# Kernel optimization log

Measured on AMD Instinct MI355X. Metric: run time of the kernel, lower is better.

Reference implementation:

```python
import jax, jax.numpy as jnp
import numpy as np

VOCAB = 50257
D_MODEL = 768
N_LAYERS = 4
N_HEADS = 12
D_HEAD = D_MODEL // N_HEADS
MAX_LEN = 5000
EPS = 1e-5


def _make_pe(max_len, d_model):
    # sinusoidal PE, interleaved sin/cos, base n=10000 (matches PositionalEncodingLayer)
    pos = jnp.arange(max_len, dtype=jnp.float32)[:, None]            # [L,1]
    i = jnp.arange(d_model // 2, dtype=jnp.float32)[None, :]         # [1,D/2]
    theta = pos / jnp.power(10000.0, 2.0 * i / d_model)              # [L,D/2]
    pe = jnp.zeros((max_len, d_model), dtype=jnp.float32)
    pe = pe.at[:, 0::2].set(jnp.sin(theta))
    pe = pe.at[:, 1::2].set(jnp.cos(theta))
    return pe


def setup_inputs() -> dict:
    key = jax.random.key(0)
    ks = jax.random.split(key, 10)
    B, S = 2, 1024
    tokens = jax.random.randint(ks[0], (B, S), 0, VOCAB)
    std = 0.02
    embed = jax.random.normal(ks[1], (VOCAB, D_MODEL), jnp.float32) * std
    pe = _make_pe(MAX_LEN, D_MODEL)
    # per-layer stacked params, torch nn.Linear convention: y = x @ W.T + b
    wq_w = jax.random.normal(ks[2], (N_LAYERS, D_MODEL, D_MODEL), jnp.float32) * std
    wk_w = jax.random.normal(ks[3], (N_LAYERS, D_MODEL, D_MODEL), jnp.float32) * std
    wv_w = jax.random.normal(ks[4], (N_LAYERS, D_MODEL, D_MODEL), jnp.float32) * std
    lin_w = jax.random.normal(ks[5], (N_LAYERS, D_MODEL, D_MODEL), jnp.float32) * std
    wq_b = jnp.zeros((N_LAYERS, D_MODEL), jnp.float32)
    wk_b = jnp.zeros((N_LAYERS, D_MODEL), jnp.float32)
    wv_b = jnp.zeros((N_LAYERS, D_MODEL), jnp.float32)
    lin_b = jnp.zeros((N_LAYERS, D_MODEL), jnp.float32)
    n1_s = jnp.ones((N_LAYERS, D_MODEL), jnp.float32)
    n1_b = jnp.zeros((N_LAYERS, D_MODEL), jnp.float32)
    n2_s = jnp.ones((N_LAYERS, D_MODEL), jnp.float32)
    n2_b = jnp.zeros((N_LAYERS, D_MODEL), jnp.float32)
    unembed_w = jax.random.normal(ks[6], (VOCAB, D_MODEL), jnp.float32) * std
    unembed_b = jnp.zeros((VOCAB,), jnp.float32)
    return dict(tokens=tokens, embed=embed, pe=pe,
                wq_w=wq_w, wq_b=wq_b, wk_w=wk_w, wk_b=wk_b, wv_w=wv_w, wv_b=wv_b,
                lin_w=lin_w, lin_b=lin_b, n1_s=n1_s, n1_b=n1_b, n2_s=n2_s, n2_b=n2_b,
                unembed_w=unembed_w, unembed_b=unembed_b)


def _layernorm(x, scale, bias):
    m = jnp.mean(x, axis=-1, keepdims=True)
    v = jnp.mean(jnp.square(x - m), axis=-1, keepdims=True)
    return (x - m) * jax.lax.rsqrt(v + EPS) * scale + bias


def _attn_block(x, wq_w, wq_b, wk_w, wk_b, wv_w, wv_b, lin_w, lin_b, n1_s, n1_b, n2_s, n2_b):
    B, S, D = x.shape
    def proj(w, b):
        y = x @ w.T + b
        return y.reshape(B, S, N_HEADS, D_HEAD).transpose(0, 2, 1, 3)  # [B,H,S,Dh]
    q, k, v = proj(wq_w, wq_b), proj(wk_w, wk_b), proj(wv_w, wv_b)
    scores = jnp.einsum('bhqd,bhkd->bhqk', q, k) / jnp.sqrt(jnp.float32(D_HEAD))
    causal = jnp.tril(jnp.ones((S, S), dtype=bool))
    scores = jnp.where(causal, scores, -jnp.inf)
    probs = jax.nn.softmax(scores, axis=-1)
    attn = jnp.einsum('bhqk,bhkd->bhqd', probs, v)
    attn = attn.transpose(0, 2, 1, 3).reshape(B, S, D)
    x = _layernorm(x + attn, n1_s, n1_b)
    x = _layernorm(x + (x @ lin_w.T + lin_b), n2_s, n2_b)
    return x


def reference(tokens, embed, pe, wq_w, wq_b, wk_w, wk_b, wv_w, wv_b,
              lin_w, lin_b, n1_s, n1_b, n2_s, n2_b, unembed_w, unembed_b):
    B, S = tokens.shape
    x = embed[tokens] + pe[:S]
    for l in range(N_LAYERS):
        x = _attn_block(x, wq_w[l], wq_b[l], wk_w[l], wk_b[l], wv_w[l], wv_b[l],
                        lin_w[l], lin_b[l], n1_s[l], n1_b[l], n2_s[l], n2_b[l])
    logits = x @ unembed_w.T + unembed_b
    return logits
```

## Files before the change

kernel.cpp:

```cpp
#include <hip/hip_runtime.h>
#include <hip/hip_bf16.h>


#define VOCAB 50257
#define DM 768
#define NL 4
#define NH 12
#define DH 64
#define SEQ 1024
#define BATCH 2
#define ROWS (BATCH * SEQ)
#define QKVN (3 * DM)

typedef __attribute__((ext_vector_type(8))) short short8;
typedef __attribute__((ext_vector_type(4))) float f32x4;

__device__ __forceinline__ unsigned short f2bf(float f) {
    union { float f; unsigned u; } v; v.f = f;
    unsigned r = v.u + 0x7FFFu + ((v.u >> 16) & 1u);
    return (unsigned short)(r >> 16);
}

#define GLOAD16(gp, lp)                                                        \
    __builtin_amdgcn_global_load_lds(                                          \
        (const __attribute__((address_space(1))) unsigned int*)(gp),           \
        (__attribute__((address_space(3))) unsigned int*)(lp), 16, 0, 0)

#define BARRIER() asm volatile("s_barrier" ::: "memory")
#define VMCNT0()  asm volatile("s_waitcnt vmcnt(0)" ::: "memory")

__global__ __launch_bounds__(256) void cvt_kernel(const float* __restrict__ in,
                                                  unsigned short* __restrict__ out,
                                                  int n4) {
    int i = blockIdx.x * 256 + threadIdx.x;
    if (i < n4) {
        float4 v = ((const float4*)in)[i];
        ushort4 o;
        o.x = f2bf(v.x); o.y = f2bf(v.y); o.z = f2bf(v.z); o.w = f2bf(v.w);
        ((ushort4*)out)[i] = o;
    }
}

__global__ __launch_bounds__(256) void cvt_qkv_kernel(const float* __restrict__ wq,
                                                      const float* __restrict__ wk,
                                                      const float* __restrict__ wv,
                                                      unsigned short* __restrict__ dst,
                                                      int n4) {
    int i = blockIdx.x * 256 + threadIdx.x;
    if (i >= n4) return;
    const int PER_L = 3 * DM * DM / 4, PER_W = DM * DM / 4;
    int l = i / PER_L;
    int rem = i - l * PER_L;
    int w = rem / PER_W;
    int r2 = rem - w * PER_W;
    const float* src = (w == 0) ? wq : (w == 1) ? wk : wv;
    float4 v = ((const float4*)src)[(size_t)l * PER_W + r2];
    ushort4 o;
    o.x = f2bf(v.x); o.y = f2bf(v.y); o.z = f2bf(v.z); o.w = f2bf(v.w);
    ((ushort4*)dst)[i] = o;
}

__global__ __launch_bounds__(256) void pack_qkv_bias(const float* __restrict__ bq,
                                                     const float* __restrict__ bk,
                                                     const float* __restrict__ bv,
                                                     float* __restrict__ dst) {
    int i = blockIdx.x * 256 + threadIdx.x;
    if (i >= NL * QKVN) return;
    int l = i / QKVN, c = i - l * QKVN;
    int w = c / DM, cc = c - w * DM;
    const float* src = (w == 0) ? bq : (w == 1) ? bk : bv;
    dst[i] = src[l * DM + cc];
}

__global__ __launch_bounds__(256) void embed_kernel(const int* __restrict__ tok,
                                                    const float* __restrict__ emb,
                                                    const float* __restrict__ pe,
                                                    float* __restrict__ xf,
                                                    unsigned short* __restrict__ xb) {
    int row = blockIdx.x;
    int t = tok[row];
    int s = row & (SEQ - 1);
    #pragma unroll
    for (int j = 0; j < 3; ++j) {
        int c = threadIdx.x + j * 256;
        float v = emb[(size_t)t * DM + c] + pe[(size_t)s * DM + c];
        xf[(size_t)row * DM + c] = v;
        xb[(size_t)row * DM + c] = f2bf(v);
    }
}

__global__ __launch_bounds__(256) void ln_kernel(const float* __restrict__ A,
                                                 const float* __restrict__ Bi,
                                                 const float* __restrict__ sc,
                                                 const float* __restrict__ bi,
                                                 float* __restrict__ xf,
                                                 unsigned short* __restrict__ xb) {
    const int w = threadIdx.x >> 6, lane = threadIdx.x & 63;
    const int row = blockIdx.x * 4 + w;
    const float* ap = A + (size_t)row * DM;
    const float* bp = Bi + (size_t)row * DM;
    float4 v[3];
    float sum = 0.f;
    #pragma unroll
    for (int j = 0; j < 3; ++j) {
        int c4 = lane * 3 + j;
        float4 a4 = ((const float4*)ap)[c4];
        float4 b4 = ((const float4*)bp)[c4];
        v[j].x = a4.x + b4.x; v[j].y = a4.y + b4.y;
        v[j].z = a4.z + b4.z; v[j].w = a4.w + b4.w;
        sum += (v[j].x + v[j].y) + (v[j].z + v[j].w);
    }
    #pragma unroll
    for (int off = 32; off > 0; off >>= 1) sum += __shfl_xor(sum, off);
    float mean = sum * (1.f / DM);
    float vs = 0.f;
    #pragma unroll
    for (int j = 0; j < 3; ++j) {
        float dx = v[j].x - mean, dy = v[j].y - mean, dz = v[j].z - mean, dw = v[j].w - mean;
        vs += dx * dx + dy * dy + dz * dz + dw * dw;
    }
    #pragma unroll
    for (int off = 32; off > 0; off >>= 1) vs += __shfl_xor(vs, off);
    float rstd = rsqrtf(vs * (1.f / DM) + 1e-5f);
    #pragma unroll
    for (int j = 0; j < 3; ++j) {
        int c4 = lane * 3 + j;
        float4 s4 = ((const float4*)sc)[c4];
        float4 b4 = ((const float4*)bi)[c4];
        float4 o;
        o.x = (v[j].x - mean) * rstd * s4.x + b4.x;
        o.y = (v[j].y - mean) * rstd * s4.y + b4.y;
        o.z = (v[j].z - mean) * rstd * s4.z + b4.z;
        o.w = (v[j].w - mean) * rstd * s4.w + b4.w;
        ((float4*)(xf + (size_t)row * DM))[c4] = o;
        ushort4 h;
        h.x = f2bf(o.x); h.y = f2bf(o.y); h.z = f2bf(o.z); h.w = f2bf(o.w);
        ((ushort4*)(xb + (size_t)row * DM))[c4] = h;
    }
}

template <int OUT_BF16>
__global__ __launch_bounds__(256, 5) void gemm64h(const unsigned short* __restrict__ A,
                                                  const unsigned short* __restrict__ B,
                                                  const float* __restrict__ bias,
                                                  void* __restrict__ C,
                                                  int M, int N, int K, int gx) {
    __shared__ __align__(16) unsigned short As[2][64 * 64];
    __shared__ __align__(16) unsigned short Bs[2][64 * 64];
    int bid = blockIdx.x;
    const int nwg = gridDim.x;
    if ((nwg & 7) == 0) {
        int q = nwg >> 3;
        bid = (bid & 7) * q + (bid >> 3);
    }
    const int bx = bid % gx, by = bid / gx;
    const int m0 = bx * 64, n0 = by * 64;
    const int tid = threadIdx.x, lane = tid & 63, wid = tid >> 6;
    const int wm = wid >> 1, wn = wid & 1;
    const int lr = lane & 15, lq = lane >> 4;

    const int sr = tid >> 3;
    const int sch = tid & 7;
    const int scs = sch ^ (sr & 7);
    const unsigned short* aP[2];
    const unsigned short* bP[2];
    int sO[2];
    #pragma unroll
    for (int i = 0; i < 2; ++i) {
        int r = sr + i * 32;
        aP[i] = A + (size_t)(m0 + r) * K + scs * 8;
        int br = n0 + r; if (br >= N) br = N - 1;
        bP[i] = B + (size_t)br * K + scs * 8;
        sO[i] = r * 64 + sch * 8;
    }

#define STG(t, c)                                                              \
    do { _Pragma("unroll")                                                     \
        for (int _i = 0; _i < 2; ++_i)                                         \
            GLOAD16(aP[_i] + (t) * 64, &As[c][sO[_i]]);                        \
        _Pragma("unroll")                                                      \
        for (int _i = 0; _i < 2; ++_i)                                         \
            GLOAD16(bP[_i] + (t) * 64, &Bs[c][sO[_i]]);                        \
    } while (0)

    f32x4 acc[2][2] = {};
    const int NT = K >> 6;

    STG(0, 0);
    VMCNT0();
    BARRIER();

    int cur = 0;
    for (int t = 0; t < NT; ++t) {
        if (t + 1 < NT) STG(t + 1, cur ^ 1);
        #pragma unroll
        for (int kk = 0; kk < 2; ++kk) {
            short8 a[2], b[2];
            #pragma unroll
            for (int i = 0; i < 2; ++i) {
                int ar = wm * 32 + i * 16 + lr;
                a[i] = *reinterpret_cast<const short8*>(
                    &As[cur][ar * 64 + (((kk * 4 + lq) ^ (ar & 7)) * 8)]);
                int br = wn * 32 + i * 16 + lr;
                b[i] = *reinterpret_cast<const short8*>(
                    &Bs[cur][br * 64 + (((kk * 4 + lq) ^ (br & 7)) * 8)]);
            }
            #pragma unroll
            for (int i = 0; i < 2; ++i)
                #pragma unroll
                for (int j = 0; j < 2; ++j)
                    acc[i][j] = __builtin_amdgcn_mfma_f32_16x16x32_bf16(a[i], b[j], acc[i][j], 0, 0, 0);
        }
        VMCNT0();
        BARRIER();
        cur ^= 1;
    }

    #pragma unroll
    for (int i = 0; i < 2; ++i) {
        int row = m0 + wm * 32 + i * 16 + lq * 4;
        #pragma unroll
        for (int j = 0; j < 2; ++j) {
            int col = n0 + wn * 32 + j * 16 + lr;
            if (col < N) {
                float bv = bias[col];
                #pragma unroll
                for (int r = 0; r < 4; ++r) {
                    float v = acc[i][j][r] + bv;
                    if (OUT_BF16) ((unsigned short*)C)[(size_t)(row + r) * N + col] = f2bf(v);
                    else          ((float*)C)[(size_t)(row + r) * N + col] = v;
                }
            }
        }
    }
#undef STG
}

__global__ __launch_bounds__(256) void attn_kernel(const unsigned short* __restrict__ Q,
                                                   const unsigned short* __restrict__ K,
                                                   const unsigned short* __restrict__ V,
                                                   int ld,
                                                   float* __restrict__ O) {
    __shared__ __align__(16) unsigned short Ks[64 * 64];
    __shared__ __align__(16) unsigned short Vs[64 * 64];
    __shared__ __align__(16) unsigned short Ps[4][16 * 64];
    const int qb = blockIdx.x;
    const int bh = blockIdx.y;
    const int b = bh / NH, h = bh % NH;
    const int tid = threadIdx.x, lane = tid & 63, w = tid >> 6;
    const int lr = lane & 15, lq = lane >> 4;
    const int wq0 = qb * 64 + w * 16;
    const size_t base = (size_t)b * SEQ * ld + h * DH;
    const size_t obase = (size_t)b * SEQ * DM + h * DH;

    short8 qf[2];
    {
        const unsigned short* qp = Q + base + (size_t)(wq0 + lr) * ld + lq * 8;
        qf[0] = *reinterpret_cast<const short8*>(qp);
        qf[1] = *reinterpret_cast<const short8*>(qp + 32);
    }
    f32x4 o_acc[4] = {};
    float mrow[4], lrow[4];
    #pragma unroll
    for (int r = 0; r < 4; ++r) { mrow[r] = -1e30f; lrow[r] = 0.f; }

    const int srow = tid >> 3, scol = (tid & 7) * 8;
    for (int t = 0; t <= qb; ++t) {
        const int kv0 = t * 64;
        #pragma unroll
        for (int rr = 0; rr < 2; ++rr) {
            int row = rr * 32 + srow;
            {
                const unsigned short* kp = K + base + (size_t)(kv0 + row) * ld + scol;
                short8 v = *reinterpret_cast<const short8*>(kp);
                *reinterpret_cast<short8*>(&Ks[(row * 64 + scol) ^ ((row & 7) << 3)]) = v;
            }
            {
                const unsigned short* vp = V + base + (size_t)(kv0 + row) * ld + scol;
                short8 v = *reinterpret_cast<const short8*>(vp);
                #pragma unroll
                for (int j = 0; j < 8; ++j) {
                    int d = scol + j;
                    Vs[(d * 64 + row) ^ ((d & 7) << 3)] = (unsigned short)v[j];
                }
            }
        }
        __syncthreads();
        if (kv0 <= wq0 + 15) {
            f32x4 s[4];
            #pragma unroll
            for (int n = 0; n < 4; ++n) {
                int br = n * 16 + lr;
                short8 b0 = *reinterpret_cast<const short8*>(&Ks[(br * 64 + lq * 8) ^ ((br & 7) << 3)]);
                short8 b1 = *reinterpret_cast<const short8*>(&Ks[(br * 64 + 32 + lq * 8) ^ ((br & 7) << 3)]);
                f32x4 z = {};
                z = __builtin_amdgcn_mfma_f32_16x16x32_bf16(qf[0], b0, z, 0, 0, 0);
                z = __builtin_amdgcn_mfma_f32_16x16x32_bf16(qf[1], b1, z, 0, 0, 0);
                s[n] = z;
            }
            const bool diag = (t == qb);
            #pragma unroll
            for (int n = 0; n < 4; ++n)
                #pragma unroll
                for (int r = 0; r < 4; ++r) {
                    float v = s[n][r] * 0.125f;
                    if (diag) {
                        int rg = wq0 + lq * 4 + r;
                        int cg = kv0 + n * 16 + lr;
                        if (cg > rg) v = -1e30f;
                    }
                    s[n][r] = v;
                }
            float f[4];
            #pragma unroll
            for (int r = 0; r < 4; ++r) {
                float mx = fmaxf(fmaxf(s[0][r], s[1][r]), fmaxf(s[2][r], s[3][r]));
                #pragma unroll
                for (int off = 1; off < 16; off <<= 1) mx = fmaxf(mx, __shfl_xor(mx, off));
                float mn = fmaxf(mrow[r], mx);
                f[r] = exp2f((mrow[r] - mn) * 1.44269504f);
                mrow[r] = mn;
            }
            #pragma unroll
            for (int n = 0; n < 4; ++n)
                #pragma unroll
                for (int r = 0; r < 4; ++r)
                    s[n][r] = exp2f((s[n][r] - mrow[r]) * 1.44269504f);
            #pragma unroll
            for (int r = 0; r < 4; ++r) {
                float ls = ((s[0][r] + s[1][r]) + (s[2][r] + s[3][r]));
                #pragma unroll
                for (int off = 1; off < 16; off <<= 1) ls += __shfl_xor(ls, off);
                lrow[r] = lrow[r] * f[r] + ls;
            }
            #pragma unroll
            for (int n = 0; n < 4; ++n)
                #pragma unroll
                for (int r = 0; r < 4; ++r) {
                    int pr = lq * 4 + r, pc = n * 16 + lr;
                    Ps[w][(pr * 64 + pc) ^ ((pr & 7) << 3)] = f2bf(s[n][r]);
                }
            #pragma unroll
            for (int n = 0; n < 4; ++n)
                #pragma unroll
                for (int r = 0; r < 4; ++r) o_acc[n][r] *= f[r];
            #pragma unroll
            for (int kk = 0; kk < 2; ++kk) {
                short8 pa = *reinterpret_cast<const short8*>(
                    &Ps[w][(lr * 64 + kk * 32 + lq * 8) ^ ((lr & 7) << 3)]);
                #pragma unroll
                for (int n = 0; n < 4; ++n) {
                    int vr = n * 16 + lr;
                    short8 bv = *reinterpret_cast<const short8*>(
                        &Vs[(vr * 64 + kk * 32 + lq * 8) ^ ((vr & 7) << 3)]);
                    o_acc[n] = __builtin_amdgcn_mfma_f32_16x16x32_bf16(pa, bv, o_acc[n], 0, 0, 0);
                }
            }
        }
        __syncthreads();
    }
    #pragma unroll
    for (int r = 0; r < 4; ++r) {
        float inv = 1.f / lrow[r];
        int row = wq0 + lq * 4 + r;
        #pragma unroll
        for (int n = 0; n < 4; ++n)
            O[obase + (size_t)row * DM + n * 16 + lr] = o_acc[n][r] * inv;
    }
}

extern "C" void kernel_launch(void* const* d_in, const int* in_sizes, int n_in,
                              void* d_out, int out_size, void* d_ws, size_t ws_size,
                              hipStream_t stream) {
    const int*   tokens   = (const int*)d_in[0];
    const float* embed    = (const float*)d_in[1];
    const float* pe       = (const float*)d_in[2];
    const float* wq_w     = (const float*)d_in[3];
    const float* wq_b     = (const float*)d_in[4];
    const float* wk_w     = (const float*)d_in[5];
    const float* wk_b     = (const float*)d_in[6];
    const float* wv_w     = (const float*)d_in[7];
    const float* wv_b     = (const float*)d_in[8];
    const float* lin_w    = (const float*)d_in[9];
    const float* lin_b    = (const float*)d_in[10];
    const float* n1_s     = (const float*)d_in[11];
    const float* n1_b     = (const float*)d_in[12];
    const float* n2_s     = (const float*)d_in[13];
    const float* n2_b     = (const float*)d_in[14];
    const float* unemb_w  = (const float*)d_in[15];
    const float* unemb_b  = (const float*)d_in[16];

    char* ws = (char*)d_ws;
    size_t off = 0;
    auto carve = [&](size_t bytes) { char* p = ws + off; off += (bytes + 255) & ~(size_t)255; return p; };
    float*          xf     = (float*)carve((size_t)ROWS * DM * 4);
    float*          yb     = (float*)carve((size_t)ROWS * DM * 4);
    unsigned short* xb     = (unsigned short*)carve((size_t)ROWS * DM * 2);
    unsigned short* qkv    = (unsigned short*)carve((size_t)ROWS * QKVN * 2);
    unsigned short* wqkv_h = (unsigned short*)carve((size_t)NL * QKVN * DM * 2);
    unsigned short* lin_h  = (unsigned short*)carve((size_t)NL * DM * DM * 2);
    unsigned short* ue_h   = (unsigned short*)carve((size_t)VOCAB * DM * 2);
    float*          qkvb   = (float*)carve((size_t)NL * QKVN * 4);

    {
        int nq4 = NL * QKVN * DM / 4;
        cvt_qkv_kernel<<<(nq4 + 255) / 256, 256, 0, stream>>>(wq_w, wk_w, wv_w, wqkv_h, nq4);
        int nl4 = NL * DM * DM / 4;
        cvt_kernel<<<(nl4 + 255) / 256, 256, 0, stream>>>(lin_w, lin_h, nl4);
        int nu4 = VOCAB * DM / 4;
        cvt_kernel<<<(nu4 + 255) / 256, 256, 0, stream>>>(unemb_w, ue_h, nu4);
        pack_qkv_bias<<<(NL * QKVN + 255) / 256, 256, 0, stream>>>(wq_b, wk_b, wv_b, qkvb);
    }
    embed_kernel<<<ROWS, 256, 0, stream>>>(tokens, embed, pe, xf, xb);

    const int gx = ROWS / 64;
    for (int l = 0; l < NL; ++l) {
        gemm64h<1><<<gx * (QKVN / 64), 256, 0, stream>>>(
            xb, wqkv_h + (size_t)l * QKVN * DM, qkvb + l * QKVN, qkv,
            ROWS, QKVN, DM, gx);
        attn_kernel<<<dim3(SEQ / 64, BATCH * NH), 256, 0, stream>>>(
            qkv, qkv + DM, qkv + 2 * DM, QKVN, yb);
        ln_kernel<<<ROWS / 4, 256, 0, stream>>>(xf, yb, n1_s + l * DM, n1_b + l * DM, xf, xb);
        gemm64h<0><<<gx * (DM / 64), 256, 0, stream>>>(
            xb, lin_h + (size_t)l * DM * DM, lin_b + l * DM, yb,
            ROWS, DM, DM, gx);
        ln_kernel<<<ROWS / 4, 256, 0, stream>>>(xf, yb, n2_s + l * DM, n2_b + l * DM, xf, xb);
    }
    const int gyu = (VOCAB + 63) / 64;
    gemm64h<0><<<gx * gyu, 256, 0, stream>>>(
        xb, ue_h, unemb_b, (float*)d_out, ROWS, VOCAB, DM, gx);
}
```

Before: 921.6 us.

## Use 128x128 tiled GEMM with 5-stage LDS pipeline for unembedding

```diff
diff --git a/kernel.cpp b/kernel.cpp
--- a/kernel.cpp
+++ b/kernel.cpp
@@ -27,6 +27,7 @@
         (__attribute__((address_space(3))) unsigned int*)(lp), 16, 0, 0)
 
 #define BARRIER() asm volatile("s_barrier" ::: "memory")
+#define VMCNT(n)  asm volatile("s_waitcnt vmcnt(" #n ")" ::: "memory")
 #define VMCNT0()  asm volatile("s_waitcnt vmcnt(0)" ::: "memory")
 
 __global__ __launch_bounds__(256) void cvt_kernel(const float* __restrict__ in,
@@ -234,6 +235,111 @@
         }
     }
 #undef STG
+}
+
+template <int OUT_BF16>
+__global__ __launch_bounds__(256, 2) void gemm128_d5(const unsigned short* __restrict__ A,
+                                                     const unsigned short* __restrict__ B,
+                                                     const float* __restrict__ bias,
+                                                     void* __restrict__ C,
+                                                     int M, int N, int K, int gx) {
+    __shared__ __align__(16) unsigned short LDS[5 * 8192];
+    int bid = blockIdx.x;
+    const int nwg = gridDim.x;
+    if ((nwg & 7) == 0) {
+        int q = nwg >> 3;
+        bid = (bid & 7) * q + (bid >> 3);
+    }
+    const int bx = bid % gx, by = bid / gx;
+    const int m0 = bx * 128, n0 = by * 128;
+    const int tid = threadIdx.x, lane = tid & 63, wid = tid >> 6;
+    const int wm = wid >> 1, wn = wid & 1;
+    const int lr = lane & 15, lq = lane >> 4;
+
+    const int srow = tid >> 2;
+    const int g = (tid & 3) ^ ((tid >> 3) & 3);
+    const unsigned short* aS[2];
+    const unsigned short* bS[2];
+    #pragma unroll
+    for (int i = 0; i < 2; ++i) {
+        int r = i * 64 + srow;
+        aS[i] = A + (size_t)(m0 + r) * K + g * 8;
+        int br = n0 + r; if (br >= N) br = N - 1;
+        bS[i] = B + (size_t)br * K + g * 8;
+    }
+
+#define STG5(t, s)                                                             \
+    do { _Pragma("unroll")                                                     \
+        for (int _i = 0; _i < 2; ++_i)                                         \
+            GLOAD16(aS[_i] + (t) * 32, &LDS[(s) * 8192 + _i * 2048 + tid * 8]);\
+        _Pragma("unroll")                                                      \
+        for (int _i = 0; _i < 2; ++_i)                                         \
+            GLOAD16(bS[_i] + (t) * 32,                                         \
+                    &LDS[(s) * 8192 + 4096 + _i * 2048 + tid * 8]);            \
+    } while (0)
+
+    int aOff[4], bOff[4];
+    #pragma unroll
+    for (int i = 0; i < 4; ++i) {
+        int ar = wm * 64 + i * 16 + lr;
+        aOff[i] = ar * 32 + ((lq ^ ((ar >> 1) & 3)) * 8);
+        int br = wn * 64 + i * 16 + lr;
+        bOff[i] = 4096 + br * 32 + ((lq ^ ((br >> 1) & 3)) * 8);
+    }
+
+    f32x4 acc[4][4] = {};
+    const int NT = K >> 5;
+
+    STG5(0, 0); STG5(1, 1); STG5(2, 2); STG5(3, 3);
+    VMCNT(12);
+    BARRIER();
+
+    int sc = 0, ss = 4;
+    #pragma unroll 1
+    for (int t = 0; t < NT; ++t) {
+        const int sb = sc * 8192;
+        short8 a[4], b[4];
+        #pragma unroll
+        for (int i = 0; i < 4; ++i) {
+            a[i] = *reinterpret_cast<const short8*>(&LDS[sb + aOff[i]]);
+            b[i] = *reinterpret_cast<const short8*>(&LDS[sb + bOff[i]]);
+        }
+        __builtin_amdgcn_s_setprio(1);
+        #pragma unroll
+        for (int i = 0; i < 4; ++i)
+            #pragma unroll
+            for (int j = 0; j < 4; ++j)
+                acc[i][j] = __builtin_amdgcn_mfma_f32_16x16x32_bf16(a[i], b[j], acc[i][j], 0, 0, 0);
+        __builtin_amdgcn_s_setprio(0);
+        BARRIER();
+        if (t + 4 < NT) STG5(t + 4, ss);
+        if (t + 4 < NT)      { VMCNT(12); }
+        else if (t + 3 < NT) { VMCNT(8); }
+        else if (t + 2 < NT) { VMCNT(4); }
+        else                 { VMCNT(0); }
+        BARRIER();
+        sc = (sc == 4) ? 0 : sc + 1;
+        ss = (ss == 4) ? 0 : ss + 1;
+    }
+
+    #pragma unroll
+    for (int i = 0; i < 4; ++i) {
+        int row = m0 + wm * 64 + i * 16 + lq * 4;
+        #pragma unroll
+        for (int j = 0; j < 4; ++j) {
+            int col = n0 + wn * 64 + j * 16 + lr;
+            if (col < N) {
+                float bv = bias[col];
+                #pragma unroll
+                for (int r = 0; r < 4; ++r) {
+                    float v = acc[i][j][r] + bv;
+                    if (OUT_BF16) ((unsigned short*)C)[(size_t)(row + r) * N + col] = f2bf(v);
+                    else          ((float*)C)[(size_t)(row + r) * N + col] = v;
+                }
+            }
+        }
+    }
+#undef STG5
 }
 
 __global__ __launch_bounds__(256) void attn_kernel(const unsigned short* __restrict__ Q,
@@ -413,20 +519,21 @@
     }
     embed_kernel<<<ROWS, 256, 0, stream>>>(tokens, embed, pe, xf, xb);
 
-    const int gx = ROWS / 64;
+    const int gx64 = ROWS / 64;
     for (int l = 0; l < NL; ++l) {
-        gemm64h<1><<<gx * (QKVN / 64), 256, 0, stream>>>(
+        gemm64h<1><<<gx64 * (QKVN / 64), 256, 0, stream>>>(
             xb, wqkv_h + (size_t)l * QKVN * DM, qkvb + l * QKVN, qkv,
-            ROWS, QKVN, DM, gx);
+            ROWS, QKVN, DM, gx64);
         attn_kernel<<<dim3(SEQ / 64, BATCH * NH), 256, 0, stream>>>(
             qkv, qkv + DM, qkv + 2 * DM, QKVN, yb);
         ln_kernel<<<ROWS / 4, 256, 0, stream>>>(xf, yb, n1_s + l * DM, n1_b + l * DM, xf, xb);
-        gemm64h<0><<<gx * (DM / 64), 256, 0, stream>>>(
+        gemm64h<0><<<gx64 * (DM / 64), 256, 0, stream>>>(
             xb, lin_h + (size_t)l * DM * DM, lin_b + l * DM, yb,
-            ROWS, DM, DM, gx);
+            ROWS, DM, DM, gx64);
         ln_kernel<<<ROWS / 4, 256, 0, stream>>>(xf, yb, n2_s + l * DM, n2_b + l * DM, xf, xb);
     }
-    const int gyu = (VOCAB + 63) / 64;
-    gemm64h<0><<<gx * gyu, 256, 0, stream>>>(
-        xb, ue_h, unemb_b, (float*)d_out, ROWS, VOCAB, DM, gx);
-}
+    const int gxu = ROWS / 128;
+    const int gyu = (VOCAB + 127) / 128;
+    gemm128_d5<0><<<gxu * gyu, 256, 0, stream>>>(
+        xb, ue_h, unemb_b, (float*)d_out, ROWS, VOCAB, DM, gxu);
+}
```

Measured after the change: 834.7 us. 9.4% less time.
